# Performance work log

Measured on AMD Instinct MI355X. Metric: run time of the kernel, lower is better.

Reference implementation:

```python
import jax, jax.numpy as jnp
import numpy as np
from jax import lax

H, W, K, B = 64, 64, 64, 64
OFFSETS = [(0, 1), (2, 1), (1, 0), (1, 2)]  # up, down, left, right slices into padded grid


def setup_inputs() -> dict:
    key = jax.random.key(0)
    ks = jax.random.split(key, 7)
    n = H * W * 3
    s = lambda d: 1.0 / np.sqrt(d)
    return {
        "obs_flat": jax.random.normal(ks[0], (B, n), jnp.float32),
        "phi_w": jax.random.normal(ks[1], (n, n), jnp.float32) * s(n),
        "phi_b": jax.random.normal(ks[2], (n,), jnp.float32) * s(n),
        "w1": jax.random.normal(ks[3], (36, 16), jnp.float32) * s(36),
        "b1": jax.random.normal(ks[4], (16,), jnp.float32) * s(36),
        "w2": jax.random.normal(ks[5], (16, 4), jnp.float32) * s(16),
        "b2": jax.random.normal(ks[6], (4,), jnp.float32) * s(16),
    }


def _vin(rin, rout, p):
    # rin, rout, p: [B, H, W]. K Bellman-style 4-neighbor sweeps.
    prin = jnp.pad(rin, ((0, 0), (1, 1), (1, 1)))
    rin_sh = jnp.stack([prin[:, ho:ho + H, wo:wo + W] for ho, wo in OFFSETS])  # [4,B,H,W]
    rout_masked = rout[None] * (rin_sh != 0).astype(rin.dtype)                 # [4,B,H,W]

    def step(V, _):
        pv = jnp.pad(V, ((0, 0), (1, 1), (1, 1)))
        v_sh = jnp.stack([pv[:, ho:ho + H, wo:wo + W] for ho, wo in OFFSETS])
        nv = p[None] * v_sh + rin_sh - rout_masked
        return jnp.maximum(V, nv.max(axis=0)), None

    V0 = jnp.zeros_like(rin)
    V, _ = lax.scan(step, V0, None, length=K)
    return V


def reference(obs_flat, phi_w, phi_b, w1, b1, w2, b2):
    obs = obs_flat.reshape(B, H, W, 3)
    phi = (obs_flat @ phi_w + phi_b).reshape(B, H, W, 3)
    rin, rout = phi[..., 0], phi[..., 1]
    p = jax.nn.softmax(phi[..., 2].reshape(B, H * W), axis=1).reshape(B, H, W)

    V = _vin(rin, rout, p)  # [B,H,W]
    obs_val = jnp.concatenate([obs, V[..., None]], axis=-1)  # [B,H,W,4]
    padded = jnp.pad(obs_val, ((0, 0), (1, 1), (1, 1), (0, 0)))

    # agent position = location of the (one-hot) nonzero in channel 1
    flat = jnp.argmax(obs[..., 1].reshape(B, -1), axis=1)
    pi, pj = flat // W, flat % W
    patch = jax.vmap(lambda x, i, j: lax.dynamic_slice(x, (i, j, 0), (3, 3, 4)))(padded, pi, pj)

    h = jax.nn.relu(patch.reshape(B, 36) @ w1 + b1)
    logit = h @ w2 + b2  # [B, 4]
    return logit
```

## Files before the change

kernel.cpp:

```cpp
#include <hip/hip_runtime.h>
#include <hip/hip_bf16.h>

typedef __attribute__((ext_vector_type(8))) short short8;
typedef __attribute__((ext_vector_type(4))) float floatx4;
typedef __attribute__((ext_vector_type(4))) unsigned short ushort4v;
typedef __attribute__((ext_vector_type(8))) unsigned short ushort8v;

#define N_DIM 12288
#define SPLITK 4
#define KCHUNK (N_DIM / SPLITK)
#define KSTEP 64
#define KITERS (KCHUNK / KSTEP)
#define NTILE 64

__device__ __forceinline__ unsigned short f2bf(float f) {
  union { float f; unsigned int i; } x; x.f = f;
  unsigned int r = x.i + 0x7fffu + ((x.i >> 16) & 1u);
  return (unsigned short)(r >> 16);
}

__global__ __launch_bounds__(256) void gemm_phi(
    const float* __restrict__ obs, const float* __restrict__ W,
    const float* __restrict__ bias, float* __restrict__ phi_part)
{
  __shared__ unsigned short A_s[2][64 * 72];
  __shared__ unsigned short W_s[2][64 * 72];

  const int t = threadIdx.x;
  const int n0 = blockIdx.x * NTILE;
  const int s  = blockIdx.y;
  const int k0 = s * KCHUNK;
  const int lane = t & 63, wv = t >> 6;
  const int l16 = lane & 15, q = lane >> 4;
  const int m0f = 16 * wv;

  const int am = t >> 2, akq = (t & 3) * 16;
  const int rg = t >> 4, cg = t & 15;

  const float* aptr = obs + (size_t)am * N_DIM + k0 + akq;
  const float* wptr = W + (size_t)(k0 + 4 * rg) * N_DIM + (n0 + 4 * cg);

  floatx4 fa0, fa1, fa2, fa3, fw0, fw1, fw2, fw3;
#define LOAD_TILE(ap, wp) do {                                              \
    fa0 = *(const floatx4*)(ap);      fa1 = *(const floatx4*)((ap) + 4);    \
    fa2 = *(const floatx4*)((ap) + 8); fa3 = *(const floatx4*)((ap) + 12);  \
    fw0 = *(const floatx4*)(wp);              fw1 = *(const floatx4*)((wp) + N_DIM); \
    fw2 = *(const floatx4*)((wp) + 2 * N_DIM); fw3 = *(const floatx4*)((wp) + 3 * N_DIM); \
  } while (0)

  LOAD_TILE(aptr, wptr);

  floatx4 acc[4];
#pragma unroll
  for (int i = 0; i < 4; i++) acc[i] = (floatx4){0.f, 0.f, 0.f, 0.f};

  for (int it = 0; it < KITERS; ++it) {
    const int cur = it & 1;
    {
      ushort8v u0, u1;
#pragma unroll
      for (int i = 0; i < 4; i++) {
        u0[i] = f2bf(fa0[i]); u0[4 + i] = f2bf(fa1[i]);
        u1[i] = f2bf(fa2[i]); u1[4 + i] = f2bf(fa3[i]);
      }
      *(ushort8v*)&A_s[cur][am * 72 + akq]     = u0;
      *(ushort8v*)&A_s[cur][am * 72 + akq + 8] = u1;
#pragma unroll
      for (int i = 0; i < 4; i++) {
        ushort4v v = { f2bf(fw0[i]), f2bf(fw1[i]), f2bf(fw2[i]), f2bf(fw3[i]) };
        *(ushort4v*)&W_s[cur][(4 * cg + i) * 72 + 4 * rg] = v;
      }
    }
    if (it + 1 < KITERS) {
      const float* ap = aptr + (it + 1) * KSTEP;
      const float* wp = wptr + (size_t)(it + 1) * KSTEP * N_DIM;
      LOAD_TILE(ap, wp);
    }
    __syncthreads();
#pragma unroll
    for (int kk = 0; kk < 2; ++kk) {
      short8 af = *(const short8*)&A_s[cur][(m0f + l16) * 72 + 32 * kk + 8 * q];
#pragma unroll
      for (int nt = 0; nt < 4; ++nt) {
        short8 wf = *(const short8*)&W_s[cur][(16 * nt + l16) * 72 + 32 * kk + 8 * q];
        acc[nt] = __builtin_amdgcn_mfma_f32_16x16x32_bf16(af, wf, acc[nt], 0, 0, 0);
      }
    }
  }

  float* dst = phi_part + (size_t)s * 64 * N_DIM;
#pragma unroll
  for (int nt = 0; nt < 4; ++nt) {
    const int ncol = n0 + 16 * nt + l16;
    const float bv = (s == 0) ? bias[ncol] : 0.f;
#pragma unroll
    for (int r = 0; r < 4; ++r) {
      const int m = m0f + q * 4 + r;
      dst[(size_t)m * N_DIM + ncol] = acc[nt][r] + bv;
    }
  }
#undef LOAD_TILE
}

#define VSTR 76
#define VOFF(h, w) (((h) + 1) * VSTR + (w) + 4)

__global__ __launch_bounds__(256) void vin_mlp(
    const float* __restrict__ obs, const float* __restrict__ phi,
    const float* __restrict__ w1, const float* __restrict__ b1,
    const float* __restrict__ w2, const float* __restrict__ b2,
    float* __restrict__ out)
{
  __shared__ float Vb[2][66 * VSTR];
  __shared__ float red_v[256];
  __shared__ int   red_i[256];

  const int b = blockIdx.x;
  const int t = threadIdx.x;
  const int ty = t >> 4, tx = t & 15;
  const int h0 = ty * 4, w0 = tx * 4;

  for (int i = t; i < 2 * 66 * VSTR; i += 256) (&Vb[0][0])[i] = 0.f;

  float rin[16], rout[16], lg[16];
#pragma unroll
  for (int r = 0; r < 4; r++) {
    const int j = 3 * ((h0 + r) * 64 + w0);
    const float* base = phi + (size_t)b * N_DIM + j;
    floatx4 x0 = *(const floatx4*)(base);
    floatx4 x1 = *(const floatx4*)(base + 4);
    floatx4 x2 = *(const floatx4*)(base + 8);
#pragma unroll
    for (int sp = 1; sp < SPLITK; sp++) {
      const float* bs = base + (size_t)sp * 64 * N_DIM;
      x0 += *(const floatx4*)(bs);
      x1 += *(const floatx4*)(bs + 4);
      x2 += *(const floatx4*)(bs + 8);
    }
    float f[12];
#pragma unroll
    for (int c = 0; c < 4; c++) { f[c] = x0[c]; f[4 + c] = x1[c]; f[8 + c] = x2[c]; }
#pragma unroll
    for (int c = 0; c < 4; c++) {
      rin [r * 4 + c] = f[3 * c + 0];
      rout[r * 4 + c] = f[3 * c + 1];
      lg  [r * 4 + c] = f[3 * c + 2];
    }
  }

  float lmax = -3.4e38f;
#pragma unroll
  for (int i = 0; i < 16; i++) lmax = fmaxf(lmax, lg[i]);
  __syncthreads();
  red_v[t] = lmax; __syncthreads();
  for (int o = 128; o > 0; o >>= 1) { if (t < o) red_v[t] = fmaxf(red_v[t], red_v[t + o]); __syncthreads(); }
  const float M = red_v[0];
  __syncthreads();
  float p[16]; float esum = 0.f;
#pragma unroll
  for (int i = 0; i < 16; i++) { p[i] = __expf(lg[i] - M); esum += p[i]; }
  red_v[t] = esum; __syncthreads();
  for (int o = 128; o > 0; o >>= 1) { if (t < o) red_v[t] += red_v[t + o]; __syncthreads(); }
  const float inv = 1.f / red_v[0];
  __syncthreads();
#pragma unroll
  for (int i = 0; i < 16; i++) p[i] *= inv;

#pragma unroll
  for (int r = 0; r < 4; r++) {
    floatx4 rr = { rin[r * 4 + 0], rin[r * 4 + 1], rin[r * 4 + 2], rin[r * 4 + 3] };
    *(floatx4*)&Vb[1][VOFF(h0 + r, w0)] = rr;
  }
  __syncthreads();
  float cu[16], cdn[16], cl[16], cr[16];
#pragma unroll
  for (int r = 0; r < 4; r++) {
#pragma unroll
    for (int c = 0; c < 4; c++) {
      const int i = r * 4 + c, h = h0 + r, w = w0 + c;
      const float nu = Vb[1][VOFF(h - 1, w)];
      const float nd = Vb[1][VOFF(h + 1, w)];
      const float nl = Vb[1][VOFF(h, w - 1)];
      const float nr = Vb[1][VOFF(h, w + 1)];
      cu [i] = nu - (nu != 0.f ? rout[i] : 0.f);
      cdn[i] = nd - (nd != 0.f ? rout[i] : 0.f);
      cl [i] = nl - (nl != 0.f ? rout[i] : 0.f);
      cr [i] = nr - (nr != 0.f ? rout[i] : 0.f);
    }
  }
  __syncthreads();

  float v[16];
#pragma unroll
  for (int i = 0; i < 16; i++) v[i] = 0.f;

  for (int k = 0; k < 64; k++) {
    const float* Vc = Vb[k & 1];
    float* Vn = Vb[(k & 1) ^ 1];
    const floatx4 top = *(const floatx4*)&Vc[VOFF(h0 - 1, w0)];
    const floatx4 bot = *(const floatx4*)&Vc[VOFF(h0 + 4, w0)];
    float lf[4], rt[4];
#pragma unroll
    for (int r = 0; r < 4; r++) { lf[r] = Vc[VOFF(h0 + r, w0 - 1)]; rt[r] = Vc[VOFF(h0 + r, w0 + 4)]; }
    float nv[16];
#pragma unroll
    for (int r = 0; r < 4; r++) {
#pragma unroll
      for (int c = 0; c < 4; c++) {
        const int i = r * 4 + c;
        const float vu = (r == 0) ? top[c] : v[i - 4];
        const float vd = (r == 3) ? bot[c] : v[i + 4];
        const float vl = (c == 0) ? lf[r] : v[i - 1];
        const float vr = (c == 3) ? rt[r] : v[i + 1];
        const float m1 = fmaxf(fmaf(p[i], vu, cu[i]), fmaf(p[i], vd, cdn[i]));
        const float m2 = fmaxf(fmaf(p[i], vl, cl[i]), fmaf(p[i], vr, cr[i]));
        nv[i] = fmaxf(v[i], fmaxf(m1, m2));
      }
    }
#pragma unroll
    for (int r = 0; r < 4; r++) {
      floatx4 w4 = { nv[r * 4 + 0], nv[r * 4 + 1], nv[r * 4 + 2], nv[r * 4 + 3] };
      *(floatx4*)&Vn[VOFF(h0 + r, w0)] = w4;
    }
#pragma unroll
    for (int i = 0; i < 16; i++) v[i] = nv[i];
    __syncthreads();
  }

  float amax = -3.4e38f; int aidx = 0;
#pragma unroll
  for (int r = 0; r < 4; r++) {
#pragma unroll
    for (int c = 0; c < 4; c++) {
      const int cell = (h0 + r) * 64 + (w0 + c);
      const float val = obs[(size_t)b * N_DIM + 3 * cell + 1];
      if (val > amax) { amax = val; aidx = cell; }
    }
  }
  red_v[t] = amax; red_i[t] = aidx;
  __syncthreads();
  for (int o = 128; o > 0; o >>= 1) {
    if (t < o) {
      const float v2 = red_v[t + o]; const int i2 = red_i[t + o];
      if (v2 > red_v[t] || (v2 == red_v[t] && i2 < red_i[t])) { red_v[t] = v2; red_i[t] = i2; }
    }
    __syncthreads();
  }
  const int pos = red_i[0];
  const int pi = pos >> 6, pj = pos & 63;
  __syncthreads();

  if (t < 36) {
    const int di = t / 12, rem = t % 12, dj = rem / 4, c4 = rem & 3;
    const int hh = pi - 1 + di, ww = pj - 1 + dj;
    float pv;
    if (c4 < 3) {
      pv = (hh >= 0 && hh < 64 && ww >= 0 && ww < 64)
           ? obs[(size_t)b * N_DIM + 3 * (hh * 64 + ww) + c4] : 0.f;
    } else {
      pv = Vb[0][VOFF(hh, ww)];
    }
    red_v[t] = pv;
  }
  __syncthreads();
  if (t < 16) {
    float a = b1[t];
#pragma unroll
    for (int j = 0; j < 36; j++) a = fmaf(red_v[j], w1[j * 16 + t], a);
    red_v[64 + t] = fmaxf(a, 0.f);
  }
  __syncthreads();
  if (t < 4) {
    float a = b2[t];
#pragma unroll
    for (int i = 0; i < 16; i++) a = fmaf(red_v[64 + i], w2[i * 4 + t], a);
    out[b * 4 + t] = a;
  }
}

extern "C" void kernel_launch(void* const* d_in, const int* in_sizes, int n_in,
                              void* d_out, int out_size, void* d_ws, size_t ws_size,
                              hipStream_t stream)
{
  (void)in_sizes; (void)n_in; (void)out_size; (void)ws_size;
  const float* obs  = (const float*)d_in[0];
  const float* phiw = (const float*)d_in[1];
  const float* phib = (const float*)d_in[2];
  const float* w1   = (const float*)d_in[3];
  const float* b1   = (const float*)d_in[4];
  const float* w2   = (const float*)d_in[5];
  const float* b2   = (const float*)d_in[6];
  float* phi = (float*)d_ws;
  float* out = (float*)d_out;

  hipLaunchKernelGGL(gemm_phi, dim3(N_DIM / NTILE, SPLITK), dim3(256), 0, stream,
                     obs, phiw, phib, phi);
  hipLaunchKernelGGL(vin_mlp, dim3(64), dim3(256), 0, stream,
                     obs, phi, w1, b1, w2, b2, out);
}
```

Before: 819.0 us.

## Deepen phi GEMM global prefetch to two tiles with manual waitcnt control

```diff
diff --git a/kernel.cpp b/kernel.cpp
--- a/kernel.cpp
+++ b/kernel.cpp
@@ -40,52 +40,63 @@
   const float* aptr = obs + (size_t)am * N_DIM + k0 + akq;
   const float* wptr = W + (size_t)(k0 + 4 * rg) * N_DIM + (n0 + 4 * cg);
 
-  floatx4 fa0, fa1, fa2, fa3, fw0, fw1, fw2, fw3;
-#define LOAD_TILE(ap, wp) do {                                              \
-    fa0 = *(const floatx4*)(ap);      fa1 = *(const floatx4*)((ap) + 4);    \
-    fa2 = *(const floatx4*)((ap) + 8); fa3 = *(const floatx4*)((ap) + 12);  \
-    fw0 = *(const floatx4*)(wp);              fw1 = *(const floatx4*)((wp) + N_DIM); \
-    fw2 = *(const floatx4*)((wp) + 2 * N_DIM); fw3 = *(const floatx4*)((wp) + 3 * N_DIM); \
+  floatx4 pa0, pa1, pa2, pa3, pw0, pw1, pw2, pw3;
+  floatx4 qa0, qa1, qa2, qa3, qw0, qw1, qw2, qw3;
+
+#define LOADS(A0, A1, A2, A3, W0, W1, W2, W3, TI) do {                       \
+    const float* ap_ = aptr + (TI) * KSTEP;                                  \
+    const float* wp_ = wptr + (size_t)(TI) * KSTEP * N_DIM;                  \
+    A0 = *(const floatx4*)(ap_);       A1 = *(const floatx4*)(ap_ + 4);      \
+    A2 = *(const floatx4*)(ap_ + 8);   A3 = *(const floatx4*)(ap_ + 12);     \
+    W0 = *(const floatx4*)(wp_);               W1 = *(const floatx4*)(wp_ + N_DIM);     \
+    W2 = *(const floatx4*)(wp_ + 2 * N_DIM);   W3 = *(const floatx4*)(wp_ + 3 * N_DIM); \
   } while (0)
 
-  LOAD_TILE(aptr, wptr);
+  LOADS(pa0, pa1, pa2, pa3, pw0, pw1, pw2, pw3, 0);
+  LOADS(qa0, qa1, qa2, qa3, qw0, qw1, qw2, qw3, 1);
 
   floatx4 acc[4];
 #pragma unroll
   for (int i = 0; i < 4; i++) acc[i] = (floatx4){0.f, 0.f, 0.f, 0.f};
 
-  for (int it = 0; it < KITERS; ++it) {
-    const int cur = it & 1;
-    {
-      ushort8v u0, u1;
-#pragma unroll
-      for (int i = 0; i < 4; i++) {
-        u0[i] = f2bf(fa0[i]); u0[4 + i] = f2bf(fa1[i]);
-        u1[i] = f2bf(fa2[i]); u1[4 + i] = f2bf(fa3[i]);
-      }
-      *(ushort8v*)&A_s[cur][am * 72 + akq]     = u0;
-      *(ushort8v*)&A_s[cur][am * 72 + akq + 8] = u1;
-#pragma unroll
-      for (int i = 0; i < 4; i++) {
-        ushort4v v = { f2bf(fw0[i]), f2bf(fw1[i]), f2bf(fw2[i]), f2bf(fw3[i]) };
-        *(ushort4v*)&W_s[cur][(4 * cg + i) * 72 + 4 * rg] = v;
-      }
-    }
-    if (it + 1 < KITERS) {
-      const float* ap = aptr + (it + 1) * KSTEP;
-      const float* wp = wptr + (size_t)(it + 1) * KSTEP * N_DIM;
-      LOAD_TILE(ap, wp);
-    }
-    __syncthreads();
-#pragma unroll
-    for (int kk = 0; kk < 2; ++kk) {
-      short8 af = *(const short8*)&A_s[cur][(m0f + l16) * 72 + 32 * kk + 8 * q];
-#pragma unroll
-      for (int nt = 0; nt < 4; ++nt) {
-        short8 wf = *(const short8*)&W_s[cur][(16 * nt + l16) * 72 + 32 * kk + 8 * q];
-        acc[nt] = __builtin_amdgcn_mfma_f32_16x16x32_bf16(af, wf, acc[nt], 0, 0, 0);
-      }
-    }
+#define STEP(TI, A0, A1, A2, A3, W0, W1, W2, W3, BUF, LAST) do {             \
+    if (LAST) asm volatile("s_waitcnt vmcnt(0)" ::: "memory");               \
+    else      asm volatile("s_waitcnt vmcnt(8)" ::: "memory");               \
+    {                                          \
+      ushort8v u0, u1;                                                       \
+      _Pragma("unroll")                                                      \
+      for (int i = 0; i < 4; i++) {                                          \
+        u0[i] = f2bf(A0[i]); u0[4 + i] = f2bf(A1[i]);                        \
+        u1[i] = f2bf(A2[i]); u1[4 + i] = f2bf(A3[i]);                        \
+      }                                                                      \
+      *(ushort8v*)&A_s[BUF][am * 72 + akq]     = u0;                         \
+      *(ushort8v*)&A_s[BUF][am * 72 + akq + 8] = u1;                         \
+      _Pragma("unroll")                                                      \
+      for (int i = 0; i < 4; i++) {                                          \
+        ushort4v v = { f2bf(W0[i]), f2bf(W1[i]), f2bf(W2[i]), f2bf(W3[i]) }; \
+        *(ushort4v*)&W_s[BUF][(4 * cg + i) * 72 + 4 * rg] = v;               \
+      }                                                                      \
+    }                                                                        \
+    if ((TI) + 2 < KITERS) {      \
+      LOADS(A0, A1, A2, A3, W0, W1, W2, W3, (TI) + 2);                       \
+    }                                                                        \
+    asm volatile("s_waitcnt lgkmcnt(0)" ::: "memory");   \
+    __builtin_amdgcn_s_barrier();                                            \
+    __builtin_amdgcn_sched_barrier(0);                                       \
+    _Pragma("unroll")                                                        \
+    for (int kk = 0; kk < 2; ++kk) {                                         \
+      short8 af = *(const short8*)&A_s[BUF][(m0f + l16) * 72 + 32 * kk + 8 * q]; \
+      _Pragma("unroll")                                                      \
+      for (int nt = 0; nt < 4; ++nt) {                                       \
+        short8 wf = *(const short8*)&W_s[BUF][(16 * nt + l16) * 72 + 32 * kk + 8 * q]; \
+        acc[nt] = __builtin_amdgcn_mfma_f32_16x16x32_bf16(af, wf, acc[nt], 0, 0, 0); \
+      }                                                                      \
+    }                                                                        \
+  } while (0)
+
+  for (int it2 = 0; it2 < KITERS; it2 += 2) {
+    STEP(it2,     pa0, pa1, pa2, pa3, pw0, pw1, pw2, pw3, 0, false);
+    STEP(it2 + 1, qa0, qa1, qa2, qa3, qw0, qw1, qw2, qw3, 1, (it2 + 1 == KITERS - 1));
   }
 
   float* dst = phi_part + (size_t)s * 64 * N_DIM;
@@ -99,7 +110,8 @@
       dst[(size_t)m * N_DIM + ncol] = acc[nt][r] + bv;
     }
   }
-#undef LOAD_TILE
+#undef STEP
+#undef LOADS
 }
 
 #define VSTR 76
```

After: 819.6 us. Within noise of the previous version (+0.1%).
